# Performance work log

Hardware: AMD Instinct MI355X
Metric: run time of the kernel (lower is better)

Reference implementation:

```python
import jax, jax.numpy as jnp
import numpy as np

LORA_ALPHA = 1
RANK = 16
SCALING = LORA_ALPHA / RANK  # self.lora_alpha / self.r


def setup_inputs() -> dict:
    key = jax.random.key(0)
    ks = jax.random.split(key, 7)
    depth, dim, r = 12, 768, 16
    B, L = 128, 197
    return {
        "x": jax.random.normal(ks[0], (B, L, dim), dtype=jnp.float32),
        "q_lora_A": jax.random.normal(ks[1], (depth, dim, r), dtype=jnp.float32) * 0.02,
        "q_lora_B": jax.random.normal(ks[2], (depth, r, dim), dtype=jnp.float32) * 0.02,
        "k_lora_A": jax.random.normal(ks[3], (depth, dim, r), dtype=jnp.float32) * 0.02,
        "k_lora_B": jax.random.normal(ks[4], (depth, r, dim), dtype=jnp.float32) * 0.02,
        "v_lora_A": jax.random.normal(ks[5], (depth, dim, r), dtype=jnp.float32) * 0.02,
        "v_lora_B": jax.random.normal(ks[6], (depth, r, dim), dtype=jnp.float32) * 0.02,
        "depth_id": 0,
    }


def reference(x, q_lora_A, q_lora_B, k_lora_A, k_lora_B, v_lora_A, v_lora_B, depth_id):
    # Faithful to MomentumLora.forward (not-old / task_id==0 branch):
    # per-depth full-rank deltas q,k,v = A[d] @ B[d]  -> each [dim, dim]
    q = q_lora_A[depth_id] @ q_lora_B[depth_id]
    k = k_lora_A[depth_id] @ k_lora_B[depth_id]
    v = v_lora_A[depth_id] @ v_lora_B[depth_id]
    # concat along last dim -> [dim, 3*dim], scale, then apply to x
    w = jnp.concatenate([q, k, v], axis=-1) * jnp.float32(SCALING)
    lora_value = jnp.einsum("bld,dz->blz", x, w)  # [B, L, 3*dim]
    return lora_value
```

## Files before the change

### kernel.cpp

```cpp
#include <hip/hip_runtime.h>


#define DIM   768
#define RNK   16
#define NCOLS 48
#define XS_STRIDE 52

typedef float f32x4 __attribute__((ext_vector_type(4)));

__global__ __launch_bounds__(192) void lora_stage1(
    const float* __restrict__ x,
    const float* __restrict__ Aq, const float* __restrict__ Ak,
    const float* __restrict__ Av,
    const int* __restrict__ depth_id,
    float* __restrict__ ypart, int kspan, int M)
{
    __shared__ float xs[128 * XS_STRIDE];
    __shared__ float as[48 * NCOLS];

    const int t  = threadIdx.x;
    const int rg = t / 12;
    const int cg = t % 12;
    const int row0  = blockIdx.x * 128;
    const int kbase = blockIdx.y * kspan;

    const int dep = depth_id[0];
    const size_t aoff = (size_t)dep * DIM * RNK;
    const float* Ab0 = Aq + aoff;
    const float* Ab1 = Ak + aoff;
    const float* Ab2 = Av + aoff;

    f32x4 acc[8] = {};

    for (int kc = 0; kc < kspan; kc += 48) {
        const int k0 = kbase + kc;
        #pragma unroll
        for (int j = 0; j < 8; j++) {
            const int f = t + j * 192;
            const int r = f / 12, k4 = f % 12;
            const f32x4 v = __builtin_nontemporal_load(
                reinterpret_cast<const f32x4*>(&x[(size_t)(row0 + r) * DIM + k0 + 4 * k4]));
            *reinterpret_cast<f32x4*>(&xs[r * XS_STRIDE + 4 * k4]) = v;
        }
        #pragma unroll
        for (int j = 0; j < 3; j++) {
            const int f = t + j * 192;
            const int k = f / 12, c4 = f % 12;
            const int z = c4 >> 2, cq = c4 & 3;
            const float* Ap = (z == 0) ? Ab0 : ((z == 1) ? Ab1 : Ab2);
            const f32x4 v = *reinterpret_cast<const f32x4*>(&Ap[(size_t)(k0 + k) * RNK + 4 * cq]);
            *reinterpret_cast<f32x4*>(&as[k * NCOLS + 4 * c4]) = v;
        }
        __syncthreads();

        #pragma unroll 2
        for (int kk = 0; kk < 48; kk += 4) {
            f32x4 xf[8], af[4];
            #pragma unroll
            for (int i = 0; i < 8; i++)
                xf[i] = *reinterpret_cast<const f32x4*>(&xs[(rg + 16 * i) * XS_STRIDE + kk]);
            #pragma unroll
            for (int j = 0; j < 4; j++)
                af[j] = *reinterpret_cast<const f32x4*>(&as[(kk + j) * NCOLS + 4 * cg]);
            #pragma unroll
            for (int i = 0; i < 8; i++) {
                acc[i] += xf[i][0] * af[0];
                acc[i] += xf[i][1] * af[1];
                acc[i] += xf[i][2] * af[2];
                acc[i] += xf[i][3] * af[3];
            }
        }
        __syncthreads();
    }

    const float s = 0.0625f;
    #pragma unroll
    for (int i = 0; i < 8; i++) {
        f32x4 v = acc[i] * s;
        *reinterpret_cast<f32x4*>(
            &ypart[((size_t)blockIdx.y * M + row0 + rg + 16 * i) * NCOLS + 4 * cg]) = v;
    }
}

__global__ __launch_bounds__(256) void lora_stage2(
    const float* __restrict__ yp,
    const float* __restrict__ Bq, const float* __restrict__ Bk,
    const float* __restrict__ Bv,
    const int* __restrict__ depth_id,
    float* __restrict__ out, int nsplit, int M)
{
    __shared__ float Bs[16 * 256];
    __shared__ float Ys[64 * 16];

    const int t    = threadIdx.x;
    const int row0 = blockIdx.x * 64;
    const int col0 = blockIdx.y * 256;
    const int z    = col0 / DIM;
    const int c0z  = col0 - z * DIM;

    const int dep = depth_id[0];
    const float* Bz = ((z == 0) ? Bq : ((z == 1) ? Bk : Bv)) + (size_t)dep * RNK * DIM;

    #pragma unroll
    for (int j = 0; j < 4; j++) {
        const int f = t + j * 256;
        const int k = f >> 6, c = f & 63;
        *reinterpret_cast<f32x4*>(&Bs[k * 256 + 4 * c]) =
            *reinterpret_cast<const f32x4*>(&Bz[(size_t)k * DIM + c0z + 4 * c]);
    }
    {
        const int r = t >> 2, q = t & 3;
        const size_t base = (size_t)(row0 + r) * NCOLS + z * RNK + 4 * q;
        f32x4 a = *reinterpret_cast<const f32x4*>(&yp[base]);
        for (int sp = 1; sp < nsplit; sp++)
            a += *reinterpret_cast<const f32x4*>(&yp[(size_t)sp * M * NCOLS + base]);
        *reinterpret_cast<f32x4*>(&Ys[r * 16 + 4 * q]) = a;
    }
    __syncthreads();

    const int w  = t >> 6;
    const int c4 = t & 63;

    f32x4 bk[16];
    #pragma unroll
    for (int k = 0; k < 16; k++)
        bk[k] = *reinterpret_cast<const f32x4*>(&Bs[k * 256 + 4 * c4]);

    #pragma unroll 2
    for (int i = 0; i < 16; i++) {
        const int r = 16 * w + i;
        const f32x4 y0 = *reinterpret_cast<const f32x4*>(&Ys[r * 16 + 0]);
        const f32x4 y1 = *reinterpret_cast<const f32x4*>(&Ys[r * 16 + 4]);
        const f32x4 y2 = *reinterpret_cast<const f32x4*>(&Ys[r * 16 + 8]);
        const f32x4 y3 = *reinterpret_cast<const f32x4*>(&Ys[r * 16 + 12]);
        f32x4 acc = y0[0] * bk[0];
        acc += y0[1] * bk[1];  acc += y0[2] * bk[2];  acc += y0[3] * bk[3];
        acc += y1[0] * bk[4];  acc += y1[1] * bk[5];  acc += y1[2] * bk[6];  acc += y1[3] * bk[7];
        acc += y2[0] * bk[8];  acc += y2[1] * bk[9];  acc += y2[2] * bk[10]; acc += y2[3] * bk[11];
        acc += y3[0] * bk[12]; acc += y3[1] * bk[13]; acc += y3[2] * bk[14]; acc += y3[3] * bk[15];
        __builtin_nontemporal_store(acc,
            reinterpret_cast<f32x4*>(&out[(size_t)(row0 + r) * (3 * DIM) + col0 + 4 * c4]));
    }
}

extern "C" void kernel_launch(void* const* d_in, const int* in_sizes, int n_in,
                              void* d_out, int out_size, void* d_ws, size_t ws_size,
                              hipStream_t stream) {
    const float* x  = (const float*)d_in[0];
    const float* Aq = (const float*)d_in[1];
    const float* Bq = (const float*)d_in[2];
    const float* Ak = (const float*)d_in[3];
    const float* Bk = (const float*)d_in[4];
    const float* Av = (const float*)d_in[5];
    const float* Bv = (const float*)d_in[6];
    const int* dep  = (const int*)d_in[7];
    float* out = (float*)d_out;
    float* y   = (float*)d_ws;

    const int M = in_sizes[0] / DIM;
    const size_t y_one = (size_t)M * NCOLS * sizeof(float);
    int nsplit = 1;
    if (ws_size >= 4 * y_one) nsplit = 4;
    else if (ws_size >= 2 * y_one) nsplit = 2;
    const int kspan = DIM / nsplit;

    lora_stage1<<<dim3(M / 128, nsplit), 192, 0, stream>>>(x, Aq, Ak, Av, dep, y, kspan, M);
    lora_stage2<<<dim3(M / 64, (3 * DIM) / 256), 256, 0, stream>>>(y, Bq, Bk, Bv, dep, out, nsplit, M);
}
```

Before: 328.3 us.

## Stash split-K partials in output row tail and compute all columns per block

Stage 1 now writes its four split-K partial products into the last 192 columns of each output row rather than a separate workspace. Stage 2 runs one block per 64 rows, which reduces the partials once into shared memory and then loops over all nine 256-column chunks, overwriting the scratch region last. The goal is to drop the workspace dependency and read and reduce y only once per row block instead of nine times. The cost is nine times fewer stage-2 blocks, serial chunk loops and B loads straight from global memory. Correctness depends on the scratch columns being overwritten only after every thread has read them, which holds because the reduction ends with a sync before the final chunk writes.

```diff
diff --git a/kernel.cpp b/kernel.cpp
--- a/kernel.cpp
+++ b/kernel.cpp
@@ -1,9 +1,13 @@
 #include <hip/hip_runtime.h>
 
 
-#define DIM   768
-#define RNK   16
-#define NCOLS 48
+#define DIM     768
+#define RNK     16
+#define NCOLS   48
+#define OUTC    2304
+#define NSPLIT  4
+#define KSPAN   192
+#define SCRATCH0 2112
 #define XS_STRIDE 52
 
 typedef float f32x4 __attribute__((ext_vector_type(4)));
@@ -13,7 +17,7 @@
     const float* __restrict__ Aq, const float* __restrict__ Ak,
     const float* __restrict__ Av,
     const int* __restrict__ depth_id,
-    float* __restrict__ ypart, int kspan, int M)
+    float* __restrict__ out)
 {
     __shared__ float xs[128 * XS_STRIDE];
     __shared__ float as[48 * NCOLS];
@@ -22,7 +26,8 @@
     const int rg = t / 12;
     const int cg = t % 12;
     const int row0  = blockIdx.x * 128;
-    const int kbase = blockIdx.y * kspan;
+    const int spl   = blockIdx.y;
+    const int kbase = spl * KSPAN;
 
     const int dep = depth_id[0];
     const size_t aoff = (size_t)dep * DIM * RNK;
@@ -32,7 +37,7 @@
 
     f32x4 acc[8] = {};
 
-    for (int kc = 0; kc < kspan; kc += 48) {
+    for (int kc = 0; kc < KSPAN; kc += 48) {
         const int k0 = kbase + kc;
         #pragma unroll
         for (int j = 0; j < 8; j++) {
@@ -78,68 +83,65 @@
     for (int i = 0; i < 8; i++) {
         f32x4 v = acc[i] * s;
         *reinterpret_cast<f32x4*>(
-            &ypart[((size_t)blockIdx.y * M + row0 + rg + 16 * i) * NCOLS + 4 * cg]) = v;
+            &out[(size_t)(row0 + rg + 16 * i) * OUTC + SCRATCH0 + spl * NCOLS + 4 * cg]) = v;
     }
 }
 
 __global__ __launch_bounds__(256) void lora_stage2(
-    const float* __restrict__ yp,
     const float* __restrict__ Bq, const float* __restrict__ Bk,
     const float* __restrict__ Bv,
     const int* __restrict__ depth_id,
-    float* __restrict__ out, int nsplit, int M)
+    float* out)
 {
-    __shared__ float Bs[16 * 256];
-    __shared__ float Ys[64 * 16];
+    __shared__ float Ys[64 * NCOLS];
 
     const int t    = threadIdx.x;
     const int row0 = blockIdx.x * 64;
-    const int col0 = blockIdx.y * 256;
-    const int z    = col0 / DIM;
-    const int c0z  = col0 - z * DIM;
-
-    const int dep = depth_id[0];
-    const float* Bz = ((z == 0) ? Bq : ((z == 1) ? Bk : Bv)) + (size_t)dep * RNK * DIM;
 
     #pragma unroll
-    for (int j = 0; j < 4; j++) {
+    for (int j = 0; j < 3; j++) {
         const int f = t + j * 256;
-        const int k = f >> 6, c = f & 63;
-        *reinterpret_cast<f32x4*>(&Bs[k * 256 + 4 * c]) =
-            *reinterpret_cast<const f32x4*>(&Bz[(size_t)k * DIM + c0z + 4 * c]);
-    }
-    {
-        const int r = t >> 2, q = t & 3;
-        const size_t base = (size_t)(row0 + r) * NCOLS + z * RNK + 4 * q;
-        f32x4 a = *reinterpret_cast<const f32x4*>(&yp[base]);
-        for (int sp = 1; sp < nsplit; sp++)
-            a += *reinterpret_cast<const f32x4*>(&yp[(size_t)sp * M * NCOLS + base]);
-        *reinterpret_cast<f32x4*>(&Ys[r * 16 + 4 * q]) = a;
+        const int r = f / 12, q4 = f % 12;
+        const size_t base = (size_t)(row0 + r) * OUTC + SCRATCH0 + 4 * q4;
+        f32x4 a = *reinterpret_cast<const f32x4*>(&out[base]);
+        #pragma unroll
+        for (int sp = 1; sp < NSPLIT; sp++)
+            a += *reinterpret_cast<const f32x4*>(&out[base + sp * NCOLS]);
+        *reinterpret_cast<f32x4*>(&Ys[r * NCOLS + 4 * q4]) = a;
     }
     __syncthreads();
 
-    const int w  = t >> 6;
-    const int c4 = t & 63;
+    const int dep = depth_id[0];
+    const int w   = t >> 6;
+    const int c4  = t & 63;
 
-    f32x4 bk[16];
-    #pragma unroll
-    for (int k = 0; k < 16; k++)
-        bk[k] = *reinterpret_cast<const f32x4*>(&Bs[k * 256 + 4 * c4]);
+    for (int chunk = 0; chunk < 9; chunk++) {
+        const int z    = chunk / 3;
+        const int c0z  = (chunk - 3 * z) * 256;
+        const int col0 = z * DIM + c0z;
+        const float* Bz = ((z == 0) ? Bq : ((z == 1) ? Bk : Bv)) + (size_t)dep * RNK * DIM;
 
-    #pragma unroll 2
-    for (int i = 0; i < 16; i++) {
-        const int r = 16 * w + i;
-        const f32x4 y0 = *reinterpret_cast<const f32x4*>(&Ys[r * 16 + 0]);
-        const f32x4 y1 = *reinterpret_cast<const f32x4*>(&Ys[r * 16 + 4]);
-        const f32x4 y2 = *reinterpret_cast<const f32x4*>(&Ys[r * 16 + 8]);
-        const f32x4 y3 = *reinterpret_cast<const f32x4*>(&Ys[r * 16 + 12]);
-        f32x4 acc = y0[0] * bk[0];
-        acc += y0[1] * bk[1];  acc += y0[2] * bk[2];  acc += y0[3] * bk[3];
-        acc += y1[0] * bk[4];  acc += y1[1] * bk[5];  acc += y1[2] * bk[6];  acc += y1[3] * bk[7];
-        acc += y2[0] * bk[8];  acc += y2[1] * bk[9];  acc += y2[2] * bk[10]; acc += y2[3] * bk[11];
-        acc += y3[0] * bk[12]; acc += y3[1] * bk[13]; acc += y3[2] * bk[14]; acc += y3[3] * bk[15];
-        __builtin_nontemporal_store(acc,
-            reinterpret_cast<f32x4*>(&out[(size_t)(row0 + r) * (3 * DIM) + col0 + 4 * c4]));
+        f32x4 bk[16];
+        #pragma unroll
+        for (int k = 0; k < 16; k++)
+            bk[k] = *reinterpret_cast<const f32x4*>(&Bz[(size_t)k * DIM + c0z + 4 * c4]);
+
+        #pragma unroll 2
+        for (int i = 0; i < 16; i++) {
+            const int r = 16 * w + i;
+            const float* yr = &Ys[r * NCOLS + z * RNK];
+            const f32x4 y0 = *reinterpret_cast<const f32x4*>(&yr[0]);
+            const f32x4 y1 = *reinterpret_cast<const f32x4*>(&yr[4]);
+            const f32x4 y2 = *reinterpret_cast<const f32x4*>(&yr[8]);
+            const f32x4 y3 = *reinterpret_cast<const f32x4*>(&yr[12]);
+            f32x4 acc = y0[0] * bk[0];
+            acc += y0[1] * bk[1];  acc += y0[2] * bk[2];  acc += y0[3] * bk[3];
+            acc += y1[0] * bk[4];  acc += y1[1] * bk[5];  acc += y1[2] * bk[6];  acc += y1[3] * bk[7];
+            acc += y2[0] * bk[8];  acc += y2[1] * bk[9];  acc += y2[2] * bk[10]; acc += y2[3] * bk[11];
+            acc += y3[0] * bk[12]; acc += y3[1] * bk[13]; acc += y3[2] * bk[14]; acc += y3[3] * bk[15];
+            __builtin_nontemporal_store(acc,
+                reinterpret_cast<f32x4*>(&out[(size_t)(row0 + r) * OUTC + col0 + 4 * c4]));
+        }
     }
 }
 
@@ -155,15 +157,10 @@
     const float* Bv = (const float*)d_in[6];
     const int* dep  = (const int*)d_in[7];
     float* out = (float*)d_out;
-    float* y   = (float*)d_ws;
+    (void)d_ws; (void)ws_size;
 
     const int M = in_sizes[0] / DIM;
-    const size_t y_one = (size_t)M * NCOLS * sizeof(float);
-    int nsplit = 1;
-    if (ws_size >= 4 * y_one) nsplit = 4;
-    else if (ws_size >= 2 * y_one) nsplit = 2;
-    const int kspan = DIM / nsplit;
 
-    lora_stage1<<<dim3(M / 128, nsplit), 192, 0, stream>>>(x, Aq, Ak, Av, dep, y, kspan, M);
-    lora_stage2<<<dim3(M / 64, (3 * DIM) / 256), 256, 0, stream>>>(y, Bq, Bk, Bv, dep, out, nsplit, M);
+    lora_stage1<<<dim3(M / 128, NSPLIT), 192, 0, stream>>>(x, Aq, Ak, Av, dep, out);
+    lora_stage2<<<dim3(M / 64), 256, 0, stream>>>(Bq, Bk, Bv, dep, out);
 }
```

New measurement: 339.3 us. 1.03x slower.
